# Kernel optimization log

Hardware: AMD Instinct MI355X
Metric: run time of the kernel (lower is better)

Reference implementation:

```python
import jax, jax.numpy as jnp
import numpy as np

D_OUT = 256  # out_channels; fourier dim F = D_OUT (Wr has F/2 rows)

def _fourier_pos(H, W, Wr, w1, b1, w2, b2):
    # normalized (H,W) grid in [-1,1], shape [L,2]
    ys = jnp.linspace(-1.0, 1.0, H)
    xs = jnp.linspace(-1.0, 1.0, W)
    gy, gx = jnp.meshgrid(ys, xs, indexing='ij')
    grid = jnp.stack([gy, gx], axis=-1).reshape(-1, 2)  # [L,2]
    proj = grid @ Wr.T                                   # [L,F/2]
    F = 2 * Wr.shape[0]
    feats = jnp.concatenate([jnp.cos(proj), jnp.sin(proj)], axis=-1) / jnp.sqrt(jnp.float32(F))
    h = jax.nn.gelu(feats @ w1.T + b1)
    return h @ w2.T + b2                                 # [L,D_OUT]

def setup_inputs() -> dict:
    key = jax.random.key(0)
    ks = jax.random.split(key, 11)
    N, D, H, W = 16, 256, 128, 128
    s = 1.0 / np.sqrt(D)
    return {
        'x': jax.random.normal(ks[0], (N, D, H, W), jnp.float32),
        'query': jax.random.normal(ks[1], (D_OUT,), jnp.float32),
        'k_w': jax.random.normal(ks[2], (D_OUT, D), jnp.float32) * s,
        'k_b': jax.random.normal(ks[3], (D_OUT,), jnp.float32) * 0.01,
        'v_w': jax.random.normal(ks[4], (D_OUT, D), jnp.float32) * s,
        'v_b': jax.random.normal(ks[5], (D_OUT,), jnp.float32) * 0.01,
        'Wr': jax.random.normal(ks[6], (D_OUT // 2, 2), jnp.float32),
        'w1': jax.random.normal(ks[7], (D_OUT, D_OUT), jnp.float32) * (1.0 / np.sqrt(D_OUT)),
        'b1': jax.random.normal(ks[8], (D_OUT,), jnp.float32) * 0.01,
        'w2': jax.random.normal(ks[9], (D_OUT, D_OUT), jnp.float32) * (1.0 / np.sqrt(D_OUT)),
        'b2': jax.random.normal(ks[10], (D_OUT,), jnp.float32) * 0.01,
    }

def reference(x, query, k_w, k_b, v_w, v_b, Wr, w1, b1, w2, b2):
    N, D, H, W = x.shape
    L = H * W
    tok = x.reshape(N, D, L).transpose(0, 2, 1)          # [N,L,D]
    pos = _fourier_pos(H, W, Wr, w1, b1, w2, b2)         # [L,D_OUT]
    K = tok @ k_w.T + k_b + pos[None]                    # [N,L,D_OUT]
    V = tok @ v_w.T + v_b                                # [N,L,D_OUT]
    scores = jnp.einsum('nld,d->nl', K, query) / jnp.sqrt(jnp.float32(query.shape[0]))
    attn = jax.nn.softmax(scores, axis=1)                # [N,L]
    return jnp.einsum('nl,nld->nd', attn, V)             # [N,D_OUT]
```

## Files before the change

### kernel.cpp

```cpp
#include <hip/hip_runtime.h>
#include <math.h>

#define NB 16
#define DD 256
#define LL 16384
#define DO 256

#define WS_QKP   0
#define WS_QW2P  2048
#define WS_W1T   4096
#define WS_VWT   (WS_W1T + 65536)
#define WS_M     (WS_VWT + 65536)
#define WS_DEN   (WS_M + NB*512)
#define WS_NUM   (WS_DEN + NB*512)

__device__ __forceinline__ float gelu_tanh(float u) {
    float u3 = u*u*u;
    return 0.5f*u*(1.0f + tanhf(0.7978845608028654f*(u + 0.044715f*u3)));
}

#define LGKMBAR() do {                                          \
    asm volatile("s_waitcnt lgkmcnt(0)" ::: "memory");          \
    __builtin_amdgcn_s_barrier();                               \
    asm volatile("" ::: "memory");                              \
} while (0)

__global__ __launch_bounds__(256) void k0(const float* __restrict__ query,
        const float* __restrict__ k_w, const float* __restrict__ w2,
        const float* __restrict__ w1, const float* __restrict__ v_w,
        float* __restrict__ ws) {
    int t = threadIdx.x, b = blockIdx.x;
    if (b < 16) {
        bool is_k = (b < 8);
        int c = b & 7;
        const float* M = is_k ? k_w : w2;
        float a = 0.f;
        #pragma unroll
        for (int oi = 0; oi < 32; ++oi) {
            int o = c*32 + oi;
            a += M[o*DD + t] * query[o];
        }
        ws[(is_k ? WS_QKP : WS_QW2P) + c*256 + t] = a;
    } else if (b < 272) {
        int f = b - 16;
        ws[WS_W1T + f*DO + t] = w1[t*DO + f];
    } else {
        int d = b - 272;
        ws[WS_VWT + d*DO + t] = v_w[t*DD + d];
    }
}

__global__ __launch_bounds__(256) void k2_fused(const float* __restrict__ x,
        const float* __restrict__ Wr, const float* __restrict__ b1,
        float* __restrict__ ws) {
    __shared__ __align__(16) float featsT[256*36];
    __shared__ float qk_s[DD];
    __shared__ float pq_s[32];
    __shared__ __align__(16) float part[128];
    __shared__ __align__(16) float e_s[32];
    int t = threadIdx.x;
    int lb = blockIdx.x;
    int l0 = lb * 32;
    int w = t >> 6, lane = t & 63;
    int dld = t >> 3, li4 = (t & 7) * 4;
    const float* xb = x + l0 + li4;

    float4 vb[2][8];
    #pragma unroll
    for (int i2 = 0; i2 < 8; ++i2)
        vb[0][i2] = *(const float4*)(xb + ((size_t)(0*DD + i2*32 + dld))*LL);
    #pragma unroll
    for (int i2 = 0; i2 < 8; ++i2)
        vb[1][i2] = *(const float4*)(xb + ((size_t)(1*DD + i2*32 + dld))*LL);

    float aqk = 0.f;
    #pragma unroll
    for (int c = 0; c < 8; ++c) aqk += ws[WS_QKP + c*256 + t];
    qk_s[t] = aqk;

    {
        int r = t & 127;
        float wr0 = Wr[r*2], wr1 = Wr[r*2+1];
        bool is_cos = (t < 128);
        #pragma unroll 8
        for (int lr = 0; lr < 32; ++lr) {
            int l = l0 + lr;
            int i = l >> 7, j = l & 127;
            float y = -1.0f + (2.0f/127.0f)*(float)i;
            float xg = -1.0f + (2.0f/127.0f)*(float)j;
            float p = y*wr0 + xg*wr1;
            featsT[t*36 + lr] = (is_cos ? cosf(p) : sinf(p)) * 0.0625f;
        }
    }
    LGKMBAR();

    float z[8][4];
    #pragma unroll
    for (int a = 0; a < 8; ++a) { z[a][0]=0.f; z[a][1]=0.f; z[a][2]=0.f; z[a][3]=0.f; }
    int o4 = lane * 4;
    const float* w1p = ws + WS_W1T + o4;
    const float* frp = featsT + w*8;
    #pragma unroll 4
    for (int f = 0; f < 256; ++f) {
        float4 wv = *(const float4*)(w1p + f*256);
        float4 fa = *(const float4*)(frp + f*36);
        float4 fbq = *(const float4*)(frp + f*36 + 4);
        float fv[8] = {fa.x,fa.y,fa.z,fa.w,fbq.x,fbq.y,fbq.z,fbq.w};
        #pragma unroll
        for (int lr = 0; lr < 8; ++lr) {
            z[lr][0] += fv[lr]*wv.x; z[lr][1] += fv[lr]*wv.y;
            z[lr][2] += fv[lr]*wv.z; z[lr][3] += fv[lr]*wv.w;
        }
    }
    {
        float4 qwv; qwv.x=0.f; qwv.y=0.f; qwv.z=0.f; qwv.w=0.f;
        #pragma unroll
        for (int c = 0; c < 8; ++c) {
            float4 p = *(const float4*)(ws + WS_QW2P + c*256 + o4);
            qwv.x += p.x; qwv.y += p.y; qwv.z += p.z; qwv.w += p.w;
        }
        float4 b1v = *(const float4*)(b1 + o4);
        #pragma unroll
        for (int lr = 0; lr < 8; ++lr) {
            float pp = gelu_tanh(z[lr][0]+b1v.x)*qwv.x + gelu_tanh(z[lr][1]+b1v.y)*qwv.y
                     + gelu_tanh(z[lr][2]+b1v.z)*qwv.z + gelu_tanh(z[lr][3]+b1v.w)*qwv.w;
            #pragma unroll
            for (int off = 32; off > 0; off >>= 1) pp += __shfl_xor(pp, off);
            if (lane == 0) pq_s[w*8 + lr] = pp;
        }
    }
    LGKMBAR();

    float qkr[8];
    #pragma unroll
    for (int i2 = 0; i2 < 8; ++i2) qkr[i2] = qk_s[i2*32 + dld];

    #pragma unroll
    for (int n = 0; n < 16; ++n) {
        const float4 (&vc)[8] = vb[n & 1];
        float sp0=0.f, sp1=0.f, sp2=0.f, sp3=0.f;
        #pragma unroll
        for (int i2 = 0; i2 < 8; ++i2) {
            sp0 += vc[i2].x * qkr[i2];
            sp1 += vc[i2].y * qkr[i2];
            sp2 += vc[i2].z * qkr[i2];
            sp3 += vc[i2].w * qkr[i2];
        }
        sp0 += __shfl_xor(sp0, 8); sp0 += __shfl_xor(sp0, 16); sp0 += __shfl_xor(sp0, 32);
        sp1 += __shfl_xor(sp1, 8); sp1 += __shfl_xor(sp1, 16); sp1 += __shfl_xor(sp1, 32);
        sp2 += __shfl_xor(sp2, 8); sp2 += __shfl_xor(sp2, 16); sp2 += __shfl_xor(sp2, 32);
        sp3 += __shfl_xor(sp3, 8); sp3 += __shfl_xor(sp3, 16); sp3 += __shfl_xor(sp3, 32);
        if (lane < 8) {
            float4 s4; s4.x=sp0; s4.y=sp1; s4.z=sp2; s4.w=sp3;
            *(float4*)(part + w*32 + li4) = s4;
        }
        LGKMBAR();
        if (t < 32) {
            float dot = part[t] + part[32+t] + part[64+t] + part[96+t];
            float score = (dot + pq_s[t]) * 0.0625f;
            float mc = score;
            #pragma unroll
            for (int off = 16; off > 0; off >>= 1) mc = fmaxf(mc, __shfl_xor(mc, off));
            float e = expf(score - mc);
            e_s[t] = e;
            float dc = e;
            #pragma unroll
            for (int off = 16; off > 0; off >>= 1) dc += __shfl_xor(dc, off);
            if (t == 0) {
                ws[WS_M + n*512 + lb] = mc;
                ws[WS_DEN + n*512 + lb] = dc;
            }
        }
        LGKMBAR();
        float4 e4 = *(const float4*)(e_s + li4);
        float na[8];
        #pragma unroll
        for (int i2 = 0; i2 < 8; ++i2)
            na[i2] = e4.x*vc[i2].x + e4.y*vc[i2].y + e4.z*vc[i2].z + e4.w*vc[i2].w;
        #pragma unroll
        for (int i2 = 0; i2 < 8; ++i2) {
            na[i2] += __shfl_xor(na[i2], 1);
            na[i2] += __shfl_xor(na[i2], 2);
            na[i2] += __shfl_xor(na[i2], 4);
        }
        if ((t & 7) == 0) {
            #pragma unroll
            for (int i2 = 0; i2 < 8; ++i2)
                ws[WS_NUM + ((size_t)n*512 + lb)*256 + i2*32 + dld] = na[i2];
        }
        if (n + 2 < 16) {
            #pragma unroll
            for (int i2 = 0; i2 < 8; ++i2)
                vb[n & 1][i2] = *(const float4*)(xb
                    + ((size_t)((n+2)*DD + i2*32 + dld))*LL);
        }
    }
}

__global__ __launch_bounds__(256) void k3_final(const float* __restrict__ ws,
        const float* __restrict__ v_b, float* __restrict__ out) {
    __shared__ float red[256];
    __shared__ float e_sc[512];
    __shared__ float s_s[DD];
    __shared__ __align__(16) float sp[4*256];
    int t = threadIdx.x, n = blockIdx.x >> 2, oq = blockIdx.x & 3;
    const float* Mp = ws + WS_M + n*512;
    const float* Dp = ws + WS_DEN + n*512;
    float m0 = Mp[t], m1 = Mp[t+256];
    red[t] = fmaxf(m0, m1);
    __syncthreads();
    for (int s = 128; s > 0; s >>= 1) {
        if (t < s) red[t] = fmaxf(red[t], red[t+s]);
        __syncthreads();
    }
    float m = red[0];
    __syncthreads();
    float e0 = expf(m0 - m), e1 = expf(m1 - m);
    e_sc[t] = e0; e_sc[t+256] = e1;
    red[t] = Dp[t]*e0 + Dp[t+256]*e1;
    __syncthreads();
    for (int s = 128; s > 0; s >>= 1) {
        if (t < s) red[t] += red[t+s];
        __syncthreads();
    }
    float den = red[0];
    __syncthreads();
    int w = t >> 6, lane = t & 63;
    const float* NBp = ws + WS_NUM + (size_t)n*512*256;
    float ax=0.f, ay=0.f, az=0.f, aw=0.f;
    #pragma unroll 4
    for (int i = 0; i < 128; ++i) {
        int lbq = w*128 + i;
        float sc = e_sc[lbq];
        float4 v4 = *(const float4*)(NBp + (size_t)lbq*256 + lane*4);
        ax += sc*v4.x; ay += sc*v4.y; az += sc*v4.z; aw += sc*v4.w;
    }
    { float4 a4; a4.x=ax; a4.y=ay; a4.z=az; a4.w=aw;
      *(float4*)(sp + w*256 + lane*4) = a4; }
    __syncthreads();
    s_s[t] = (sp[t] + sp[256+t] + sp[512+t] + sp[768+t]) / den;
    __syncthreads();
    int o = oq*64 + lane;
    float acc = 0.f;
    #pragma unroll 8
    for (int i = 0; i < 64; ++i) {
        int d = w*64 + i;
        acc += ws[WS_VWT + d*DO + o] * s_s[d];
    }
    red[t] = acc;
    __syncthreads();
    if (t < 64)
        out[n*DO + oq*64 + t] = v_b[oq*64 + t]
            + red[t] + red[64+t] + red[128+t] + red[192+t];
}

extern "C" void kernel_launch(void* const* d_in, const int* in_sizes, int n_in,
                              void* d_out, int out_size, void* d_ws, size_t ws_size,
                              hipStream_t stream) {
    const float* x     = (const float*)d_in[0];
    const float* query = (const float*)d_in[1];
    const float* k_w   = (const float*)d_in[2];
    const float* v_w   = (const float*)d_in[4];
    const float* v_b   = (const float*)d_in[5];
    const float* Wr    = (const float*)d_in[6];
    const float* w1    = (const float*)d_in[7];
    const float* b1    = (const float*)d_in[8];
    const float* w2    = (const float*)d_in[9];
    float* ws  = (float*)d_ws;
    float* out = (float*)d_out;

    k0<<<528, 256, 0, stream>>>(query, k_w, w2, w1, v_w, ws);
    k2_fused<<<512, 256, 0, stream>>>(x, Wr, b1, ws);
    k3_final<<<64, 256, 0, stream>>>(ws, v_b, out);
}
```

Before: 434.4 us.

## Fold final softmax reduction into main kernel via last-blocks atomic ticket

```diff
diff --git a/kernel.cpp b/kernel.cpp
--- a/kernel.cpp
+++ b/kernel.cpp
@@ -13,6 +13,7 @@
 #define WS_M     (WS_VWT + 65536)
 #define WS_DEN   (WS_M + NB*512)
 #define WS_NUM   (WS_DEN + NB*512)
+#define WS_CNT   (WS_NUM + NB*512*256)
 
 __device__ __forceinline__ float gelu_tanh(float u) {
     float u3 = u*u*u;
@@ -30,6 +31,7 @@
         const float* __restrict__ w1, const float* __restrict__ v_w,
         float* __restrict__ ws) {
     int t = threadIdx.x, b = blockIdx.x;
+    if (b == 0 && t == 0) *(unsigned*)(ws + WS_CNT) = 0u;
     if (b < 16) {
         bool is_k = (b < 8);
         int c = b & 7;
@@ -50,14 +52,16 @@
     }
 }
 
-__global__ __launch_bounds__(256) void k2_fused(const float* __restrict__ x,
+__global__ __launch_bounds__(256, 2) void k2_fused(const float* __restrict__ x,
         const float* __restrict__ Wr, const float* __restrict__ b1,
+        const float* __restrict__ v_b, float* __restrict__ out,
         float* __restrict__ ws) {
     __shared__ __align__(16) float featsT[256*36];
     __shared__ float qk_s[DD];
     __shared__ float pq_s[32];
     __shared__ __align__(16) float part[128];
     __shared__ __align__(16) float e_s[32];
+    __shared__ unsigned ticket_s;
     int t = threadIdx.x;
     int lb = blockIdx.x;
     int l0 = lb * 32;
@@ -65,6 +69,10 @@
     int dld = t >> 3, li4 = (t & 7) * 4;
     const float* xb = x + l0 + li4;
 
+    float qp[8];
+    #pragma unroll
+    for (int c = 0; c < 8; ++c) qp[c] = ws[WS_QKP + c*256 + t];
+
     float4 vb[2][8];
     #pragma unroll
     for (int i2 = 0; i2 < 8; ++i2)
@@ -73,9 +81,7 @@
     for (int i2 = 0; i2 < 8; ++i2)
         vb[1][i2] = *(const float4*)(xb + ((size_t)(1*DD + i2*32 + dld))*LL);
 
-    float aqk = 0.f;
-    #pragma unroll
-    for (int c = 0; c < 8; ++c) aqk += ws[WS_QKP + c*256 + t];
+    float aqk = qp[0]+qp[1]+qp[2]+qp[3]+qp[4]+qp[5]+qp[6]+qp[7];
     qk_s[t] = aqk;
 
     {
@@ -195,17 +201,25 @@
                     + ((size_t)((n+2)*DD + i2*32 + dld))*LL);
         }
     }
-}
-
-__global__ __launch_bounds__(256) void k3_final(const float* __restrict__ ws,
-        const float* __restrict__ v_b, float* __restrict__ out) {
-    __shared__ float red[256];
-    __shared__ float e_sc[512];
-    __shared__ float s_s[DD];
-    __shared__ __align__(16) float sp[4*256];
-    int t = threadIdx.x, n = blockIdx.x >> 2, oq = blockIdx.x & 3;
-    const float* Mp = ws + WS_M + n*512;
-    const float* Dp = ws + WS_DEN + n*512;
+
+    __threadfence();
+    if (t == 0) ticket_s = atomicAdd((unsigned*)(ws + WS_CNT), 1u);
+    __syncthreads();
+    unsigned ticket = ticket_s;
+    if (ticket < 496u) return;
+    int nn = (int)ticket - 496;
+    if (t == 0) {
+        while (atomicAdd((unsigned*)(ws + WS_CNT), 0u) < 512u)
+            __builtin_amdgcn_s_sleep(2);
+    }
+    __syncthreads();
+    __threadfence();
+    float* red  = featsT;
+    float* e_sc = featsT + 256;
+    float* s_s  = featsT + 768;
+    float* spb  = featsT + 1024;
+    const float* Mp = ws + WS_M + nn*512;
+    const float* Dp = ws + WS_DEN + nn*512;
     float m0 = Mp[t], m1 = Mp[t+256];
     red[t] = fmaxf(m0, m1);
     __syncthreads();
@@ -225,8 +239,7 @@
     }
     float den = red[0];
     __syncthreads();
-    int w = t >> 6, lane = t & 63;
-    const float* NBp = ws + WS_NUM + (size_t)n*512*256;
+    const float* NBp = ws + WS_NUM + (size_t)nn*512*256;
     float ax=0.f, ay=0.f, az=0.f, aw=0.f;
     #pragma unroll 4
     for (int i = 0; i < 128; ++i) {
@@ -236,22 +249,15 @@
         ax += sc*v4.x; ay += sc*v4.y; az += sc*v4.z; aw += sc*v4.w;
     }
     { float4 a4; a4.x=ax; a4.y=ay; a4.z=az; a4.w=aw;
-      *(float4*)(sp + w*256 + lane*4) = a4; }
-    __syncthreads();
-    s_s[t] = (sp[t] + sp[256+t] + sp[512+t] + sp[768+t]) / den;
-    __syncthreads();
-    int o = oq*64 + lane;
-    float acc = 0.f;
+      *(float4*)(spb + w*256 + lane*4) = a4; }
+    __syncthreads();
+    s_s[t] = (spb[t] + spb[256+t] + spb[512+t] + spb[768+t]) / den;
+    __syncthreads();
+    float acc = v_b[t];
     #pragma unroll 8
-    for (int i = 0; i < 64; ++i) {
-        int d = w*64 + i;
-        acc += ws[WS_VWT + d*DO + o] * s_s[d];
-    }
-    red[t] = acc;
-    __syncthreads();
-    if (t < 64)
-        out[n*DO + oq*64 + t] = v_b[oq*64 + t]
-            + red[t] + red[64+t] + red[128+t] + red[192+t];
+    for (int d = 0; d < 256; ++d)
+        acc += ws[WS_VWT + d*DO + t] * s_s[d];
+    out[nn*DO + t] = acc;
 }
 
 extern "C" void kernel_launch(void* const* d_in, const int* in_sizes, int n_in,
@@ -270,6 +276,5 @@
     float* out = (float*)d_out;
 
     k0<<<528, 256, 0, stream>>>(query, k_w, w2, w1, v_w, ws);
-    k2_fused<<<512, 256, 0, stream>>>(x, Wr, b1, ws);
-    k3_final<<<64, 256, 0, stream>>>(ws, v_b, out);
-}
+    k2_fused<<<512, 256, 0, stream>>>(x, Wr, b1, v_b, out, ws);
+}
```

New measurement: 522.5 us. 1.2x slower.
